# Optimization experiments

Measured on AMD Instinct MI355X. Metric: run time of the kernel, lower is better.

## Reference

```python
import jax, jax.numpy as jnp
import numpy as np

K_MASK = -2.3819763e+38
ROTARY_DIM = 80        # int(128 * 0.625), already even
ROPE_THETA = 1000000.0
NORM_EPS = 1e-6


def apply_rope(x, positions, head_dim, rope_theta):
    # x: [B, T, n, head_dim]; positions: [B, T]
    fraction = 2.0 * jnp.arange(0, head_dim // 2, dtype=jnp.float32) / head_dim
    timescale = rope_theta ** fraction                      # [hd/2]
    sinusoid = positions.astype(jnp.float32)[..., None] / timescale[None, None, :]
    sinusoid = sinusoid[..., None, :]                       # [B, T, 1, hd/2]
    sin = jnp.sin(sinusoid).astype(x.dtype)
    cos = jnp.cos(sinusoid).astype(x.dtype)
    first, second = jnp.split(x, 2, axis=-1)
    return jnp.concatenate(
        [first * cos - second * sin, second * cos + first * sin], axis=-1
    ).astype(x.dtype)


def rms_norm(x, w, eps=NORM_EPS):
    # Qwen3.5 convention: x/rms * (1 + w), w zero-initialized
    out = x * jax.lax.rsqrt(jnp.mean(x * x, axis=-1, keepdims=True) + eps)
    return out * (1.0 + w)


def setup_inputs() -> dict:
    B, T, D, N, K, H = 4, 1024, 4096, 32, 8, 128
    key = jax.random.key(0)
    ks = jax.random.split(key, 5)
    return {
        "x": jax.random.normal(ks[0], (B, T, D), jnp.float32),
        "positions": jnp.tile(jnp.arange(T, dtype=jnp.int32)[None, :], (B, 1)),
        "wq": jax.random.normal(ks[1], (D, N, 2 * H), jnp.float32) * 0.02,
        "wk": jax.random.normal(ks[2], (D, K, H), jnp.float32) * 0.02,
        "wv": jax.random.normal(ks[3], (D, K, H), jnp.float32) * 0.02,
        "wo": jax.random.normal(ks[4], (N, H, D), jnp.float32) * 0.02,
        "q_norm_w": jnp.zeros((H,), jnp.float32),
        "k_norm_w": jnp.zeros((H,), jnp.float32),
    }


def reference(x, positions, wq, wk, wv, wo, q_norm_w, k_norm_w):
    H = wk.shape[-1]
    # QKV projections; q_proj produces head_dim*2 -> (query, sigmoid gate)
    qg = jnp.einsum('BTD,DNH->BTNH', x, wq)            # [B,T,N,2H]
    q, gate = jnp.split(qg, 2, axis=-1)                # [B,T,N,H] each
    k = jnp.einsum('BSD,DKH->BSKH', x, wk)             # [B,S,K,H]
    v = jnp.einsum('BSD,DKH->BSKH', x, wv)             # [B,S,K,H]
    # per-head RMSNorm (Qwen3.5 style)
    q = rms_norm(q, q_norm_w)
    k = rms_norm(k, k_norm_w)
    # partial RoPE on first ROTARY_DIM dims of each head
    q = jnp.concatenate(
        [apply_rope(q[..., :ROTARY_DIM], positions, ROTARY_DIM, ROPE_THETA),
         q[..., ROTARY_DIM:]], axis=-1)
    k = jnp.concatenate(
        [apply_rope(k[..., :ROTARY_DIM], positions, ROTARY_DIM, ROPE_THETA),
         k[..., ROTARY_DIM:]], axis=-1)
    B, T, N, _ = q.shape
    Kh = k.shape[2]
    G = N // Kh                                        # GQA group size
    qg5 = q.reshape(B, T, Kh, G, H)
    scores = jnp.einsum('BTKGH,BSKH->BKGTS', qg5, k) * (H ** -0.5)
    causal = jnp.tril(jnp.ones((T, T), dtype=bool))    # [T,S]
    scores = jnp.where(causal[None, None, None, :, :], scores, K_MASK)
    probs = jax.nn.softmax(scores, axis=-1)
    out = jnp.einsum('BKGTS,BSKH->BTKGH', probs, v).reshape(B, T, N, H)
    out = out * jax.nn.sigmoid(gate)                   # gated attention output
    return jnp.einsum('BTNH,NHD->BTD', out, wo)
```

## Files before the change

kernel.cpp:

```cpp
#include <hip/hip_runtime.h>
#include <cstdint>
#include <cstddef>


typedef __attribute__((ext_vector_type(8))) short short8;
typedef __attribute__((ext_vector_type(4))) float float4v;

__device__ __forceinline__ unsigned short f2bf(float f) {
  unsigned u = __builtin_bit_cast(unsigned, f);
  u += 0x7fffu + ((u >> 16) & 1u);
  return (unsigned short)(u >> 16);
}
__device__ __forceinline__ float bf2f(unsigned short h) {
  unsigned u = ((unsigned)h) << 16;
  return __builtin_bit_cast(float, u);
}

__device__ __forceinline__ void gload_lds16(const void* g, void* l) {
  typedef const __attribute__((address_space(1))) void as1_cv;
  typedef __attribute__((address_space(3))) void as3_v;
  __builtin_amdgcn_global_load_lds((as1_cv*)g, (as3_v*)l, 16, 0, 0);
}

__global__ __launch_bounds__(256) void transpose_cvt(
    const float* __restrict__ src, unsigned short* __restrict__ dst,
    int R, int C) {
  __shared__ float tile[32][33];
  const int c0 = blockIdx.x * 32, r0 = blockIdx.y * 32;
  for (int i = threadIdx.y; i < 32; i += 8)
    tile[i][threadIdx.x] = src[(size_t)(r0 + i) * C + c0 + threadIdx.x];
  __syncthreads();
  for (int i = threadIdx.y; i < 32; i += 8)
    dst[(size_t)(c0 + i) * R + r0 + threadIdx.x] = f2bf(tile[threadIdx.x][i]);
}

__global__ __launch_bounds__(256) void cvt_f32_bf16(
    const float* __restrict__ src, unsigned short* __restrict__ dst, int n4) {
  int i = blockIdx.x * blockDim.x + threadIdx.x;
  if (i >= n4) return;
  float4 f = ((const float4*)src)[i];
  ushort4 o;
  o.x = f2bf(f.x); o.y = f2bf(f.y); o.z = f2bf(f.z); o.w = f2bf(f.w);
  ((ushort4*)dst)[i] = o;
}

__global__ __launch_bounds__(256) void v_transpose(
    const unsigned short* __restrict__ qkv, unsigned short* __restrict__ vtb) {
  __shared__ unsigned short tile[64][65];
  const int t0 = blockIdx.x * 64, h0 = blockIdx.y * 64;
  const int bk = blockIdx.z, b = bk >> 3, kh = bk & 7;
  const int tx = threadIdx.x & 63, ty = threadIdx.x >> 6;
  const unsigned short* src =
      qkv + (size_t)(b * 1024 + t0) * 10240 + 9216 + kh * 128 + h0;
  for (int i = ty; i < 64; i += 4)
    tile[i][tx] = src[(size_t)i * 10240 + tx];
  __syncthreads();
  unsigned short* dst = vtb + ((size_t)bk * 128 + h0) * 1024 + t0;
  for (int i = ty; i < 64; i += 4)
    dst[(size_t)i * 1024 + tx] = tile[tx][i];
}

template <bool BF16OUT>
__global__ __launch_bounds__(512, 2) void gemm_bt256(
    const unsigned short* __restrict__ A, const unsigned short* __restrict__ BT,
    void* __restrict__ Cv, int M, int N, int Kd) {
  __shared__ unsigned short As[2][16384];
  __shared__ unsigned short Bs[2][16384];

  const int tid = threadIdx.x;
  const int lane = tid & 63;
  const int wv = tid >> 6;
  const int wr = wv >> 2, wc = wv & 3;
  const int m0 = blockIdx.y * 256, n0 = blockIdx.x * 256;
  const int ml = lane & 15, q = lane >> 4;

  const int srow = tid >> 3;
  const int sgc = ((tid & 7) ^ (srow & 7)) * 8;
  const unsigned short* gA = A + (size_t)(m0 + srow) * Kd + sgc;
  const unsigned short* gB = BT + (size_t)(n0 + srow) * Kd + sgc;
  const int ldst = tid * 8;

  const int rch = (q ^ (ml & 7)) * 8;
  const int aBase = (wr * 128 + ml) * 64 + rch;
  const int bBase = (wc * 64 + ml) * 64 + rch;

  float4v acc[8][4];
#pragma unroll
  for (int i = 0; i < 8; ++i)
#pragma unroll
    for (int j = 0; j < 4; ++j) acc[i][j] = (float4v)0.0f;

  const int NT = Kd >> 6;

#pragma unroll
  for (int h = 0; h < 4; ++h) {
    const unsigned short* g = (h < 2) ? gA : gB;
    const int hr = (h & 1) * 128;
    unsigned short* l = (h < 2) ? &As[0][(h & 1) * 8192] : &Bs[0][(h & 1) * 8192];
    gload_lds16(g + (size_t)hr * Kd, l + ldst);
    gload_lds16(g + (size_t)(hr + 64) * Kd, l + ldst + 4096);
  }
  asm volatile("s_waitcnt vmcnt(0)" ::: "memory");
  __builtin_amdgcn_s_barrier();

#pragma unroll 2
  for (int T = 0; T < NT; ++T) {
    const unsigned short* Ab = As[T & 1];
    const unsigned short* Bb = Bs[T & 1];
    const bool doStage = (T + 1 < NT);

    short8 af[8], ba[4], bb[4];
#pragma unroll
    for (int i = 0; i < 4; ++i) {
      af[i * 2]     = *(const short8*)&Ab[aBase + i * 1024];
      af[i * 2 + 1] = *(const short8*)&Ab[(aBase + i * 1024) ^ 32];
    }
#pragma unroll
    for (int j = 0; j < 2; ++j) {
      ba[j * 2]     = *(const short8*)&Bb[bBase + j * 1024];
      ba[j * 2 + 1] = *(const short8*)&Bb[(bBase + j * 1024) ^ 32];
    }
    __builtin_amdgcn_sched_barrier(0);
#pragma unroll
    for (int j = 0; j < 2; ++j) {
      bb[j * 2]     = *(const short8*)&Bb[bBase + 2048 + j * 1024];
      bb[j * 2 + 1] = *(const short8*)&Bb[(bBase + 2048 + j * 1024) ^ 32];
    }
    asm volatile("s_waitcnt lgkmcnt(4)" ::: "memory");
    __builtin_amdgcn_sched_barrier(0);
    __builtin_amdgcn_s_setprio(1);
#pragma unroll
    for (int i = 0; i < 4; ++i)
#pragma unroll
      for (int j = 0; j < 2; ++j) {
        acc[i][j] = __builtin_amdgcn_mfma_f32_16x16x32_bf16(af[i * 2], ba[j * 2], acc[i][j], 0, 0, 0);
        acc[i][j] = __builtin_amdgcn_mfma_f32_16x16x32_bf16(af[i * 2 + 1], ba[j * 2 + 1], acc[i][j], 0, 0, 0);
      }
    __builtin_amdgcn_s_setprio(0);
    __builtin_amdgcn_s_barrier();

    asm volatile("s_waitcnt lgkmcnt(0)" ::: "memory");
    __builtin_amdgcn_sched_barrier(0);
    __builtin_amdgcn_s_setprio(1);
#pragma unroll
    for (int i = 0; i < 4; ++i)
#pragma unroll
      for (int j = 0; j < 2; ++j) {
        acc[i][2 + j] = __builtin_amdgcn_mfma_f32_16x16x32_bf16(af[i * 2], bb[j * 2], acc[i][2 + j], 0, 0, 0);
        acc[i][2 + j] = __builtin_amdgcn_mfma_f32_16x16x32_bf16(af[i * 2 + 1], bb[j * 2 + 1], acc[i][2 + j], 0, 0, 0);
      }
    __builtin_amdgcn_s_setprio(0);
    __builtin_amdgcn_s_barrier();

#pragma unroll
    for (int i = 0; i < 4; ++i) {
      af[i * 2]     = *(const short8*)&Ab[aBase + 4096 + i * 1024];
      af[i * 2 + 1] = *(const short8*)&Ab[(aBase + 4096 + i * 1024) ^ 32];
    }
    __builtin_amdgcn_sched_barrier(0);
    if (doStage) {
      const int sb = (T + 1) & 1;
      const size_t kk = (size_t)(T + 1) * 64;
#pragma unroll
      for (int h = 0; h < 4; ++h) {
        const unsigned short* g = (h < 2) ? gA : gB;
        const int hr = (h & 1) * 128;
        unsigned short* l = (h < 2) ? &As[sb][(h & 1) * 8192] : &Bs[sb][(h & 1) * 8192];
        gload_lds16(g + (size_t)hr * Kd + kk, l + ldst);
        gload_lds16(g + (size_t)(hr + 64) * Kd + kk, l + ldst + 4096);
      }
    }
    asm volatile("s_waitcnt lgkmcnt(0)" ::: "memory");
    __builtin_amdgcn_sched_barrier(0);
    __builtin_amdgcn_s_setprio(1);
#pragma unroll
    for (int i = 0; i < 4; ++i)
#pragma unroll
      for (int j = 0; j < 2; ++j) {
        acc[4 + i][j] = __builtin_amdgcn_mfma_f32_16x16x32_bf16(af[i * 2], ba[j * 2], acc[4 + i][j], 0, 0, 0);
        acc[4 + i][j] = __builtin_amdgcn_mfma_f32_16x16x32_bf16(af[i * 2 + 1], ba[j * 2 + 1], acc[4 + i][j], 0, 0, 0);
      }
    __builtin_amdgcn_s_setprio(0);
    __builtin_amdgcn_s_barrier();

    __builtin_amdgcn_s_setprio(1);
#pragma unroll
    for (int i = 0; i < 4; ++i)
#pragma unroll
      for (int j = 0; j < 2; ++j) {
        acc[4 + i][2 + j] = __builtin_amdgcn_mfma_f32_16x16x32_bf16(af[i * 2], bb[j * 2], acc[4 + i][2 + j], 0, 0, 0);
        acc[4 + i][2 + j] = __builtin_amdgcn_mfma_f32_16x16x32_bf16(af[i * 2 + 1], bb[j * 2 + 1], acc[4 + i][2 + j], 0, 0, 0);
      }
    __builtin_amdgcn_s_setprio(0);
    if (doStage)
      asm volatile("s_waitcnt vmcnt(0)" ::: "memory");
    __builtin_amdgcn_s_barrier();
  }

#pragma unroll
  for (int i = 0; i < 8; ++i) {
#pragma unroll
    for (int j = 0; j < 4; ++j) {
      const int grow = m0 + wr * 128 + i * 16 + q * 4;
      const int gcol = n0 + wc * 64 + j * 16 + ml;
#pragma unroll
      for (int r = 0; r < 4; ++r) {
        size_t idx = (size_t)(grow + r) * N + gcol;
        if constexpr (BF16OUT)
          ((unsigned short*)Cv)[idx] = f2bf(acc[i][j][r]);
        else
          ((float*)Cv)[idx] = acc[i][j][r];
      }
    }
  }
}

__global__ __launch_bounds__(256) void postproc_kernel(
    const unsigned short* __restrict__ qkv, const int* __restrict__ positions,
    const float* __restrict__ qnw, const float* __restrict__ knw,
    unsigned short* __restrict__ q_rot, unsigned short* __restrict__ sgb,
    unsigned short* __restrict__ k_rot) {
  const int wave = threadIdx.x >> 6, lane = threadIdx.x & 63;
  const int gslot = blockIdx.x * 4 + wave;
  const int m = gslot / 40, hs = gslot % 40;
  const int b = m >> 10, t = m & 1023;

  const unsigned short* base = (hs < 32)
      ? qkv + (size_t)m * 10240 + hs * 256
      : qkv + (size_t)m * 10240 + 8192 + (hs - 32) * 128;

  float v1 = bf2f(base[lane]);
  float v2 = bf2f(base[64 + lane]);

  float ss = v1 * v1 + v2 * v2;
  for (int off = 32; off > 0; off >>= 1) ss += __shfl_xor(ss, off);
  const float r = rsqrtf(ss * (1.0f / 128.0f) + 1e-6f);
  const float* nw = (hs < 32) ? qnw : knw;
  v1 *= r * (1.0f + nw[lane]);
  v2 *= r * (1.0f + nw[64 + lane]);

  const float pos = (float)positions[m];
  const int i1 = (lane < 40) ? lane : lane - 40;
  const float ang1 = pos * expf(-0.3453877639491068f * (float)i1);
  const float s1 = sinf(ang1), c1 = cosf(ang1);
  const float ang2 = pos * expf(-0.3453877639491068f * (float)(lane + 24));
  const float s2 = sinf(ang2), c2 = cosf(ang2);

  const float shA1 = __shfl(v1, (lane + 40) & 63);
  const float shA2 = __shfl(v2, (lane + 40) & 63);
  const float shX = __shfl(v1, (lane + 24) & 63);
  const float pA = (lane < 24) ? shA1 : shA2;
  const float o1 = (lane < 40) ? (v1 * c1 - pA * s1) : (v1 * c1 + shX * s1);
  const float o2 = (lane < 16) ? (v2 * c2 + shX * s2) : v2;

  if (hs < 32) {
    size_t qb = ((size_t)m * 32 + hs) * 128;
    q_rot[qb + lane] = f2bf(o1);
    q_rot[qb + 64 + lane] = f2bf(o2);
    float g1 = bf2f(base[128 + lane]), g2 = bf2f(base[192 + lane]);
    sgb[qb + lane] = f2bf(1.0f / (1.0f + expf(-g1)));
    sgb[qb + 64 + lane] = f2bf(1.0f / (1.0f + expf(-g2)));
  } else {
    const int kh = hs - 32;
    size_t kb = ((size_t)(b * 8 + kh) * 1024 + t) * 128;
    k_rot[kb + lane] = f2bf(o1);
    k_rot[kb + 64 + lane] = f2bf(o2);
  }
}

__global__ __launch_bounds__(256) void attn_kernel(
    const unsigned short* __restrict__ q_rot, const unsigned short* __restrict__ k_rot,
    const unsigned short* __restrict__ vt, const unsigned short* __restrict__ sgate,
    unsigned short* __restrict__ attn_out) {
  __shared__ unsigned short Ks[64 * 128];
  __shared__ unsigned short Vts[128 * 64];
  __shared__ unsigned short Ps[64 * 72];

  const int tid = threadIdx.x;
  const int lane = tid & 63, w = tid >> 6;
  const int qt = blockIdx.x & 15;
  const int n = (blockIdx.x >> 4) & 31;
  const int b = blockIdx.x >> 9;
  const int kh = n >> 2;
  const int t0 = qt * 64;
  const int ml = lane & 15, q = lane >> 4;
  const float SCALE = 0.08838834764831845f;

  short8 aq[4];
  {
    const unsigned short* qp =
        q_rot + (((size_t)(b * 1024 + t0 + w * 16 + ml)) * 32 + n) * 128 + q * 8;
#pragma unroll
    for (int ks = 0; ks < 4; ++ks) aq[ks] = *(const short8*)(qp + ks * 32);
  }

  float4v O[8];
#pragma unroll
  for (int i = 0; i < 8; ++i) O[i] = (float4v)0.0f;
  float mrow[4] = {-3e38f, -3e38f, -3e38f, -3e38f};
  float lrow[4] = {0.f, 0.f, 0.f, 0.f};

  const unsigned short* kbase = k_rot + (size_t)(b * 8 + kh) * 1024 * 128;
  const unsigned short* vbase = vt + (size_t)(b * 8 + kh) * 128 * 1024;
  const int rK = tid >> 4, cK = tid & 15;
  const int cKsw = (cK ^ rK) * 8;
  const int rV = tid >> 3, cV = tid & 7;
  const int cVsw = (cV ^ (rV & 7)) * 8;

  for (int si = 0; si <= qt; ++si) {
    const int s0 = si * 64;
#pragma unroll
    for (int it = 0; it < 4; ++it) {
      const int li = it * 256 + tid;
      gload_lds16(kbase + (size_t)(s0 + rK + it * 16) * 128 + cKsw, &Ks[li * 8]);
      gload_lds16(vbase + (size_t)(rV + it * 32) * 1024 + s0 + cVsw, &Vts[li * 8]);
    }
    __syncthreads();

    float4v Sv[4];
#pragma unroll
    for (int j = 0; j < 4; ++j) Sv[j] = (float4v)0.0f;
#pragma unroll
    for (int ks = 0; ks < 4; ++ks) {
#pragma unroll
      for (int j = 0; j < 4; ++j) {
        short8 bk = *(const short8*)&Ks[(j * 16 + ml) * 128 + (((ks * 4 + q) ^ ml) * 8)];
        Sv[j] = __builtin_amdgcn_mfma_f32_16x16x32_bf16(aq[ks], bk, Sv[j], 0, 0, 0);
      }
    }

    float P[4][4];
#pragma unroll
    for (int rr = 0; rr < 4; ++rr) {
      const int tg = t0 + w * 16 + q * 4 + rr;
      float vmax = -3e38f;
#pragma unroll
      for (int j = 0; j < 4; ++j) {
        const int sj = s0 + j * 16 + ml;
        float v = Sv[j][rr] * SCALE;
        if (sj > tg) v = -3.0e38f;
        P[j][rr] = v;
        vmax = fmaxf(vmax, v);
      }
      for (int off = 1; off < 16; off <<= 1) vmax = fmaxf(vmax, __shfl_xor(vmax, off));
      const float mnew = fmaxf(mrow[rr], vmax);
      const float alpha = __expf(mrow[rr] - mnew);
      mrow[rr] = mnew;
      lrow[rr] *= alpha;
#pragma unroll
      for (int ht = 0; ht < 8; ++ht) O[ht][rr] *= alpha;
      float rsum = 0.f;
#pragma unroll
      for (int j = 0; j < 4; ++j) {
        float e = __expf(P[j][rr] - mnew);
        P[j][rr] = e;
        rsum += e;
      }
      for (int off = 1; off < 16; off <<= 1) rsum += __shfl_xor(rsum, off);
      lrow[rr] += rsum;
    }

#pragma unroll
    for (int rr = 0; rr < 4; ++rr)
#pragma unroll
      for (int j = 0; j < 4; ++j)
        Ps[(w * 16 + q * 4 + rr) * 72 + j * 16 + ml] = f2bf(P[j][rr]);

#pragma unroll
    for (int ks = 0; ks < 2; ++ks) {
      short8 ap = *(const short8*)&Ps[(w * 16 + ml) * 72 + ks * 32 + q * 8];
#pragma unroll
      for (int ht = 0; ht < 8; ++ht) {
        short8 bv = *(const short8*)&Vts[(ht * 16 + ml) * 64 + (((ks * 4 + q) ^ (ml & 7)) * 8)];
        O[ht] = __builtin_amdgcn_mfma_f32_16x16x32_bf16(ap, bv, O[ht], 0, 0, 0);
      }
    }
    __syncthreads();
  }

#pragma unroll
  for (int rr = 0; rr < 4; ++rr) {
    const int tg = t0 + w * 16 + q * 4 + rr;
    const size_t ob = ((size_t)(b * 1024 + tg) * 32 + n) * 128;
    const float inv = 1.0f / lrow[rr];
#pragma unroll
    for (int ht = 0; ht < 8; ++ht) {
      const int h = ht * 16 + ml;
      attn_out[ob + h] = f2bf(O[ht][rr] * inv * bf2f(sgate[ob + h]));
    }
  }
}

extern "C" void kernel_launch(void* const* d_in, const int* in_sizes, int n_in,
                              void* d_out, int out_size, void* d_ws, size_t ws_size,
                              hipStream_t stream) {
  (void)in_sizes; (void)n_in; (void)out_size; (void)ws_size;
  const float* x = (const float*)d_in[0];
  const int* pos = (const int*)d_in[1];
  const float* wq = (const float*)d_in[2];
  const float* wk = (const float*)d_in[3];
  const float* wv = (const float*)d_in[4];
  const float* wo = (const float*)d_in[5];
  const float* qnw = (const float*)d_in[6];
  const float* knw = (const float*)d_in[7];
  float* out = (float*)d_out;

  unsigned short* ws = (unsigned short*)d_ws;
  unsigned short* x_bf = ws;
  unsigned short* wT = x_bf + 16777216;
  unsigned short* woT = wT + 41943040;
  unsigned short* qkv = woT + 16777216;
  unsigned short* q_rot = qkv + 41943040;
  unsigned short* sgb = q_rot + 16777216;
  unsigned short* k_rot = sgb + 16777216;
  unsigned short* vtb = k_rot + 4194304;
  unsigned short* attn = wT;

  dim3 tb(32, 8);
  transpose_cvt<<<dim3(256, 128), tb, 0, stream>>>(wq, wT, 4096, 8192);
  transpose_cvt<<<dim3(32, 128), tb, 0, stream>>>(wk, wT + (size_t)8192 * 4096, 4096, 1024);
  transpose_cvt<<<dim3(32, 128), tb, 0, stream>>>(wv, wT + (size_t)9216 * 4096, 4096, 1024);
  transpose_cvt<<<dim3(128, 128), tb, 0, stream>>>(wo, woT, 4096, 4096);
  cvt_f32_bf16<<<16384, 256, 0, stream>>>(x, x_bf, 4194304);

  gemm_bt256<true><<<dim3(40, 16), 512, 0, stream>>>(x_bf, wT, (void*)qkv, 4096, 10240, 4096);
  postproc_kernel<<<40960, 256, 0, stream>>>(qkv, pos, qnw, knw, q_rot, sgb, k_rot);
  v_transpose<<<dim3(16, 2, 32), 256, 0, stream>>>(qkv, vtb);
  attn_kernel<<<2048, 256, 0, stream>>>(q_rot, k_rot, vtb, sgb, attn);
  gemm_bt256<false><<<dim3(16, 16), 512, 0, stream>>>(attn, woT, (void*)out, 4096, 4096, 4096);
}
```

Before: 1.093 ms.

## Double-buffer attention K/V loads, merge prep kernels, precompute RoPE table

The attention kernel now double-buffers K and V tiles in LDS. It issues the next tile's global-to-LDS loads before computing on the current one, using explicit vmcnt waits and raw barriers instead of __syncthreads. The four weight transposes and the x conversion are merged into one prep kernel, and the V transpose is folded into the post-processing kernel, which cuts launch count. A sin/cos table is computed in double precision once per call and replaces the per-element expf/sinf/cosf in post-processing. The extra LDS for double buffering may lower attention occupancy, and the table uses extra workspace.

```diff
diff --git a/kernel.cpp b/kernel.cpp
--- a/kernel.cpp
+++ b/kernel.cpp
@@ -22,42 +22,49 @@
   __builtin_amdgcn_global_load_lds((as1_cv*)g, (as3_v*)l, 16, 0, 0);
 }
 
-__global__ __launch_bounds__(256) void transpose_cvt(
+__device__ __forceinline__ void tcvt_body(
     const float* __restrict__ src, unsigned short* __restrict__ dst,
-    int R, int C) {
+    int R, int C, int bx, int by, int tid, float (*tile)[33]) {
+  const int tx = tid & 31, ty = tid >> 5;
+  const int c0 = bx * 32, r0 = by * 32;
+  for (int i = ty; i < 32; i += 8)
+    tile[i][tx] = src[(size_t)(r0 + i) * C + c0 + tx];
+  __syncthreads();
+  for (int i = ty; i < 32; i += 8)
+    dst[(size_t)(c0 + i) * R + r0 + tx] = f2bf(tile[tx][i]);
+}
+
+__global__ __launch_bounds__(256) void prep_kernel(
+    const float* __restrict__ wq, const float* __restrict__ wk,
+    const float* __restrict__ wv, const float* __restrict__ wo,
+    const float* __restrict__ x, unsigned short* __restrict__ wT,
+    unsigned short* __restrict__ woT, unsigned short* __restrict__ x_bf,
+    float2* __restrict__ sctab) {
   __shared__ float tile[32][33];
-  const int c0 = blockIdx.x * 32, r0 = blockIdx.y * 32;
-  for (int i = threadIdx.y; i < 32; i += 8)
-    tile[i][threadIdx.x] = src[(size_t)(r0 + i) * C + c0 + threadIdx.x];
-  __syncthreads();
-  for (int i = threadIdx.y; i < 32; i += 8)
-    dst[(size_t)(c0 + i) * R + r0 + threadIdx.x] = f2bf(tile[threadIdx.x][i]);
-}
-
-__global__ __launch_bounds__(256) void cvt_f32_bf16(
-    const float* __restrict__ src, unsigned short* __restrict__ dst, int n4) {
-  int i = blockIdx.x * blockDim.x + threadIdx.x;
-  if (i >= n4) return;
-  float4 f = ((const float4*)src)[i];
-  ushort4 o;
-  o.x = f2bf(f.x); o.y = f2bf(f.y); o.z = f2bf(f.z); o.w = f2bf(f.w);
-  ((ushort4*)dst)[i] = o;
-}
-
-__global__ __launch_bounds__(256) void v_transpose(
-    const unsigned short* __restrict__ qkv, unsigned short* __restrict__ vtb) {
-  __shared__ unsigned short tile[64][65];
-  const int t0 = blockIdx.x * 64, h0 = blockIdx.y * 64;
-  const int bk = blockIdx.z, b = bk >> 3, kh = bk & 7;
-  const int tx = threadIdx.x & 63, ty = threadIdx.x >> 6;
-  const unsigned short* src =
-      qkv + (size_t)(b * 1024 + t0) * 10240 + 9216 + kh * 128 + h0;
-  for (int i = ty; i < 64; i += 4)
-    tile[i][tx] = src[(size_t)i * 10240 + tx];
-  __syncthreads();
-  unsigned short* dst = vtb + ((size_t)bk * 128 + h0) * 1024 + t0;
-  for (int i = ty; i < 64; i += 4)
-    dst[(size_t)i * 1024 + tx] = tile[tx][i];
+  const int b = blockIdx.x, tid = threadIdx.x;
+  if (b < 32768) {
+    tcvt_body(wq, wT, 4096, 8192, b & 255, b >> 8, tid, tile);
+  } else if (b < 36864) {
+    const int r = b - 32768;
+    tcvt_body(wk, wT + (size_t)8192 * 4096, 4096, 1024, r & 31, r >> 5, tid, tile);
+  } else if (b < 40960) {
+    const int r = b - 36864;
+    tcvt_body(wv, wT + (size_t)9216 * 4096, 4096, 1024, r & 31, r >> 5, tid, tile);
+  } else if (b < 57344) {
+    const int r = b - 40960;
+    tcvt_body(wo, woT, 4096, 4096, r & 127, r >> 7, tid, tile);
+  } else if (b < 73728) {
+    const int i = (b - 57344) * 256 + tid;
+    float4 f = ((const float4*)x)[i];
+    ushort4 o;
+    o.x = f2bf(f.x); o.y = f2bf(f.y); o.z = f2bf(f.z); o.w = f2bf(f.w);
+    ((ushort4*)x_bf)[i] = o;
+  } else {
+    const int e = (b - 73728) * 256 + tid;
+    const int t = e / 40, i = e - t * 40;
+    const double ang = (double)t * exp(-0.34538776394910684 * (double)i);
+    sctab[e] = make_float2((float)sin(ang), (float)cos(ang));
+  }
 }
 
 template <bool BF16OUT>
@@ -215,56 +222,76 @@
   }
 }
 
-__global__ __launch_bounds__(256) void postproc_kernel(
+__global__ __launch_bounds__(256) void post_kernel(
     const unsigned short* __restrict__ qkv, const int* __restrict__ positions,
     const float* __restrict__ qnw, const float* __restrict__ knw,
     unsigned short* __restrict__ q_rot, unsigned short* __restrict__ sgb,
-    unsigned short* __restrict__ k_rot) {
-  const int wave = threadIdx.x >> 6, lane = threadIdx.x & 63;
-  const int gslot = blockIdx.x * 4 + wave;
-  const int m = gslot / 40, hs = gslot % 40;
-  const int b = m >> 10, t = m & 1023;
-
-  const unsigned short* base = (hs < 32)
-      ? qkv + (size_t)m * 10240 + hs * 256
-      : qkv + (size_t)m * 10240 + 8192 + (hs - 32) * 128;
-
-  float v1 = bf2f(base[lane]);
-  float v2 = bf2f(base[64 + lane]);
-
-  float ss = v1 * v1 + v2 * v2;
-  for (int off = 32; off > 0; off >>= 1) ss += __shfl_xor(ss, off);
-  const float r = rsqrtf(ss * (1.0f / 128.0f) + 1e-6f);
-  const float* nw = (hs < 32) ? qnw : knw;
-  v1 *= r * (1.0f + nw[lane]);
-  v2 *= r * (1.0f + nw[64 + lane]);
-
-  const float pos = (float)positions[m];
-  const int i1 = (lane < 40) ? lane : lane - 40;
-  const float ang1 = pos * expf(-0.3453877639491068f * (float)i1);
-  const float s1 = sinf(ang1), c1 = cosf(ang1);
-  const float ang2 = pos * expf(-0.3453877639491068f * (float)(lane + 24));
-  const float s2 = sinf(ang2), c2 = cosf(ang2);
-
-  const float shA1 = __shfl(v1, (lane + 40) & 63);
-  const float shA2 = __shfl(v2, (lane + 40) & 63);
-  const float shX = __shfl(v1, (lane + 24) & 63);
-  const float pA = (lane < 24) ? shA1 : shA2;
-  const float o1 = (lane < 40) ? (v1 * c1 - pA * s1) : (v1 * c1 + shX * s1);
-  const float o2 = (lane < 16) ? (v2 * c2 + shX * s2) : v2;
-
-  if (hs < 32) {
-    size_t qb = ((size_t)m * 32 + hs) * 128;
-    q_rot[qb + lane] = f2bf(o1);
-    q_rot[qb + 64 + lane] = f2bf(o2);
-    float g1 = bf2f(base[128 + lane]), g2 = bf2f(base[192 + lane]);
-    sgb[qb + lane] = f2bf(1.0f / (1.0f + expf(-g1)));
-    sgb[qb + 64 + lane] = f2bf(1.0f / (1.0f + expf(-g2)));
+    unsigned short* __restrict__ k_rot, unsigned short* __restrict__ vtb,
+    const float2* __restrict__ sctab) {
+  __shared__ unsigned short vt_tile[64][65];
+  const int bidx = blockIdx.x;
+
+  if (bidx < 40960) {
+    const int wave = threadIdx.x >> 6, lane = threadIdx.x & 63;
+    const int gslot = bidx * 4 + wave;
+    const int m = gslot / 40, hs = gslot % 40;
+    const int b = m >> 10, t = m & 1023;
+
+    const unsigned short* base = (hs < 32)
+        ? qkv + (size_t)m * 10240 + hs * 256
+        : qkv + (size_t)m * 10240 + 8192 + (hs - 32) * 128;
+
+    float v1 = bf2f(base[lane]);
+    float v2 = bf2f(base[64 + lane]);
+
+    float ss = v1 * v1 + v2 * v2;
+    for (int off = 32; off > 0; off >>= 1) ss += __shfl_xor(ss, off);
+    const float r = rsqrtf(ss * (1.0f / 128.0f) + 1e-6f);
+    const float* nw = (hs < 32) ? qnw : knw;
+    v1 *= r * (1.0f + nw[lane]);
+    v2 *= r * (1.0f + nw[64 + lane]);
+
+    const float2* sc = sctab + (size_t)positions[m] * 40;
+    const int i1 = (lane < 40) ? lane : lane - 40;
+    const float2 sc1 = sc[i1];
+    const float2 sc2 = sc[(lane < 16) ? (lane + 24) : 0];
+    const float s1 = sc1.x, c1 = sc1.y;
+    const float s2 = sc2.x, c2 = sc2.y;
+
+    const float shA1 = __shfl(v1, (lane + 40) & 63);
+    const float shA2 = __shfl(v2, (lane + 40) & 63);
+    const float shX = __shfl(v1, (lane + 24) & 63);
+    const float pA = (lane < 24) ? shA1 : shA2;
+    const float o1 = (lane < 40) ? (v1 * c1 - pA * s1) : (v1 * c1 + shX * s1);
+    const float o2 = (lane < 16) ? (v2 * c2 + shX * s2) : v2;
+
+    if (hs < 32) {
+      size_t qb = ((size_t)m * 32 + hs) * 128;
+      q_rot[qb + lane] = f2bf(o1);
+      q_rot[qb + 64 + lane] = f2bf(o2);
+      float g1 = bf2f(base[128 + lane]), g2 = bf2f(base[192 + lane]);
+      sgb[qb + lane] = f2bf(1.0f / (1.0f + expf(-g1)));
+      sgb[qb + 64 + lane] = f2bf(1.0f / (1.0f + expf(-g2)));
+    } else {
+      const int kh = hs - 32;
+      size_t kb = ((size_t)(b * 8 + kh) * 1024 + t) * 128;
+      k_rot[kb + lane] = f2bf(o1);
+      k_rot[kb + 64 + lane] = f2bf(o2);
+    }
   } else {
-    const int kh = hs - 32;
-    size_t kb = ((size_t)(b * 8 + kh) * 1024 + t) * 128;
-    k_rot[kb + lane] = f2bf(o1);
-    k_rot[kb + 64 + lane] = f2bf(o2);
+    const int rel = bidx - 40960;
+    const int tt = rel & 15, hh = (rel >> 4) & 1, bk = rel >> 5;
+    const int t0 = tt * 64, h0 = hh * 64;
+    const int b = bk >> 3, kh = bk & 7;
+    const int tx = threadIdx.x & 63, ty = threadIdx.x >> 6;
+    const unsigned short* src =
+        qkv + (size_t)(b * 1024 + t0) * 10240 + 9216 + kh * 128 + h0;
+    for (int i = ty; i < 64; i += 4)
+      vt_tile[i][tx] = src[(size_t)i * 10240 + tx];
+    __syncthreads();
+    unsigned short* dst = vtb + ((size_t)bk * 128 + h0) * 1024 + t0;
+    for (int i = ty; i < 64; i += 4)
+      dst[(size_t)i * 1024 + tx] = vt_tile[tx][i];
   }
 }
 
@@ -272,8 +299,8 @@
     const unsigned short* __restrict__ q_rot, const unsigned short* __restrict__ k_rot,
     const unsigned short* __restrict__ vt, const unsigned short* __restrict__ sgate,
     unsigned short* __restrict__ attn_out) {
-  __shared__ unsigned short Ks[64 * 128];
-  __shared__ unsigned short Vts[128 * 64];
+  __shared__ unsigned short Ks[2][64 * 128];
+  __shared__ unsigned short Vts[2][128 * 64];
   __shared__ unsigned short Ps[64 * 72];
 
   const int tid = threadIdx.x;
@@ -307,15 +334,31 @@
   const int rV = tid >> 3, cV = tid & 7;
   const int cVsw = (cV ^ (rV & 7)) * 8;
 
+#define ATTN_STAGE(SI, BF) do {                                               \
+    const int ss0 = (SI) * 64;                                                \
+    _Pragma("unroll")                                                         \
+    for (int it = 0; it < 4; ++it) {                                          \
+      const int li = it * 256 + tid;                                          \
+      gload_lds16(kbase + (size_t)(ss0 + rK + it * 16) * 128 + cKsw,          \
+                  &Ks[BF][li * 8]);                                           \
+      gload_lds16(vbase + (size_t)(rV + it * 32) * 1024 + ss0 + cVsw,         \
+                  &Vts[BF][li * 8]);                                          \
+    } } while (0)
+
+  ATTN_STAGE(0, 0);
+
   for (int si = 0; si <= qt; ++si) {
+    const int buf = si & 1;
     const int s0 = si * 64;
-#pragma unroll
-    for (int it = 0; it < 4; ++it) {
-      const int li = it * 256 + tid;
-      gload_lds16(kbase + (size_t)(s0 + rK + it * 16) * 128 + cKsw, &Ks[li * 8]);
-      gload_lds16(vbase + (size_t)(rV + it * 32) * 1024 + s0 + cVsw, &Vts[li * 8]);
-    }
-    __syncthreads();
+    if (si < qt) {
+      ATTN_STAGE(si + 1, buf ^ 1);
+      __builtin_amdgcn_sched_barrier(0);
+      asm volatile("s_waitcnt vmcnt(8)" ::: "memory");
+    } else {
+      asm volatile("s_waitcnt vmcnt(0)" ::: "memory");
+    }
+    __builtin_amdgcn_s_barrier();
+    __builtin_amdgcn_sched_barrier(0);
 
     float4v Sv[4];
 #pragma unroll
@@ -324,7 +367,7 @@
     for (int ks = 0; ks < 4; ++ks) {
 #pragma unroll
       for (int j = 0; j < 4; ++j) {
-        short8 bk = *(const short8*)&Ks[(j * 16 + ml) * 128 + (((ks * 4 + q) ^ ml) * 8)];
+        short8 bk = *(const short8*)&Ks[buf][(j * 16 + ml) * 128 + (((ks * 4 + q) ^ ml) * 8)];
         Sv[j] = __builtin_amdgcn_mfma_f32_16x16x32_bf16(aq[ks], bk, Sv[j], 0, 0, 0);
       }
     }
@@ -371,12 +414,14 @@
       short8 ap = *(const short8*)&Ps[(w * 16 + ml) * 72 + ks * 32 + q * 8];
 #pragma unroll
       for (int ht = 0; ht < 8; ++ht) {
-        short8 bv = *(const short8*)&Vts[(ht * 16 + ml) * 64 + (((ks * 4 + q) ^ (ml & 7)) * 8)];
+        short8 bv = *(const short8*)&Vts[buf][(ht * 16 + ml) * 64 + (((ks * 4 + q) ^ (ml & 7)) * 8)];
         O[ht] = __builtin_amdgcn_mfma_f32_16x16x32_bf16(ap, bv, O[ht], 0, 0, 0);
       }
     }
-    __syncthreads();
-  }
+    __builtin_amdgcn_sched_barrier(0);
+    __builtin_amdgcn_s_barrier();
+  }
+#undef ATTN_STAGE
 
 #pragma unroll
   for (int rr = 0; rr < 4; ++rr) {
@@ -414,18 +459,12 @@
   unsigned short* sgb = q_rot + 16777216;
   unsigned short* k_rot = sgb + 16777216;
   unsigned short* vtb = k_rot + 4194304;
+  float2* sctab = (float2*)(vtb + 4194304);
   unsigned short* attn = wT;
 
-  dim3 tb(32, 8);
-  transpose_cvt<<<dim3(256, 128), tb, 0, stream>>>(wq, wT, 4096, 8192);
-  transpose_cvt<<<dim3(32, 128), tb, 0, stream>>>(wk, wT + (size_t)8192 * 4096, 4096, 1024);
-  transpose_cvt<<<dim3(32, 128), tb, 0, stream>>>(wv, wT + (size_t)9216 * 4096, 4096, 1024);
-  transpose_cvt<<<dim3(128, 128), tb, 0, stream>>>(wo, woT, 4096, 4096);
-  cvt_f32_bf16<<<16384, 256, 0, stream>>>(x, x_bf, 4194304);
-
+  prep_kernel<<<73888, 256, 0, stream>>>(wq, wk, wv, wo, x, wT, woT, x_bf, sctab);
   gemm_bt256<true><<<dim3(40, 16), 512, 0, stream>>>(x_bf, wT, (void*)qkv, 4096, 10240, 4096);
-  postproc_kernel<<<40960, 256, 0, stream>>>(qkv, pos, qnw, knw, q_rot, sgb, k_rot);
-  v_transpose<<<dim3(16, 2, 32), 256, 0, stream>>>(qkv, vtb);
+  post_kernel<<<41984, 256, 0, stream>>>(qkv, pos, qnw, knw, q_rot, sgb, k_rot, vtb, sctab);
   attn_kernel<<<2048, 256, 0, stream>>>(q_rot, k_rot, vtb, sgb, attn);
   gemm_bt256<false><<<dim3(16, 16), 512, 0, stream>>>(attn, woT, (void*)out, 4096, 4096, 4096);
 }
```

New measurement: 1.064 ms. -2.7%, faster.
